# Kernel optimization log

Hardware: AMD Instinct MI355X
Metric: run time of the kernel (lower is better)

## Reference

```python
import jax, jax.numpy as jnp
import numpy as np

B, T1, T2, V, D, H = 128, 256, 256, 50000, 300, 300


def _lstm_dir(x, lens, Wih, Whh, bih, bhh):
    # PyTorch LSTM gate order: i, f, g, o. Length-masked scan emulates pack_padded_sequence:
    # state frozen and outputs zeroed for t >= len.
    Bn, T, _ = x.shape
    Hn = Whh.shape[1]
    mask = (jnp.arange(T)[None, :] < lens[:, None]).astype(x.dtype)[..., None]  # [B,T,1]

    def step(carry, inp):
        h, c = carry
        xt, mt = inp
        gates = xt @ Wih.T + bih + h @ Whh.T + bhh
        i, f, g, o = jnp.split(gates, 4, axis=-1)
        c_new = jax.nn.sigmoid(f) * c + jax.nn.sigmoid(i) * jnp.tanh(g)
        h_new = jax.nn.sigmoid(o) * jnp.tanh(c_new)
        h = mt * h_new + (1.0 - mt) * h
        c = mt * c_new + (1.0 - mt) * c
        return (h, c), h * mt

    init = (jnp.zeros((Bn, Hn), x.dtype), jnp.zeros((Bn, Hn), x.dtype))
    _, ys = jax.lax.scan(step, init, (x.swapaxes(0, 1), mask.swapaxes(0, 1)))
    return ys.swapaxes(0, 1)  # [B,T,H]


def _bilstm(x, lens, Wf_ih, Wf_hh, bf_ih, bf_hh, Wb_ih, Wb_hh, bb_ih, bb_hh):
    out_f = _lstm_dir(x, lens, Wf_ih, Wf_hh, bf_ih, bf_hh)
    T = x.shape[1]
    t = jnp.arange(T)[None, :]
    # per-sample reversal of the valid prefix (involution): rev[t] = l-1-t for t<l else t
    idx = jnp.where(t < lens[:, None], lens[:, None] - 1 - t, t)
    xr = jnp.take_along_axis(x, idx[..., None], axis=1)
    yr = _lstm_dir(xr, lens, Wb_ih, Wb_hh, bb_ih, bb_hh)
    out_b = jnp.take_along_axis(yr, idx[..., None], axis=1)
    return jnp.concatenate([out_f, out_b], axis=-1)  # [B,T,2H]


def _bidaf_both(u1, l1, u2, l2):
    S = jnp.einsum('bid,bjd->bij', u1, u2)  # [B,t1,t2]
    v1 = jnp.arange(S.shape[1])[None, :] < l1[:, None]
    v2 = jnp.arange(S.shape[2])[None, :] < l2[:, None]
    Sm = jnp.where(v1[:, :, None] & v2[:, None, :], S, -1e9)
    # softmax over t2 (s1->s2 attention); invalid rows zeroed (matches NaN->0 fill)
    a2 = jax.nn.softmax(Sm, axis=2) * v1[:, :, None].astype(S.dtype)
    a1 = jax.nn.softmax(Sm, axis=1) * v2[:, None, :].astype(S.dtype)
    U = jnp.einsum('bij,bjd->bid', a2, u2)   # tile for s1
    U1 = jnp.einsum('bij,bid->bjd', a1, u1)  # tile for s2
    return U, U1


def _max_along_time(x, lens):
    v = jnp.arange(x.shape[1])[None, :] < lens[:, None]
    return jnp.max(jnp.where(v[:, :, None], x, -jnp.inf), axis=1)


def _forward(s1, l1, s2, l2, emb,
             w1f_ih, w1f_hh, b1f_ih, b1f_hh, w1b_ih, w1b_hh, b1b_ih, b1b_hh,
             w2f_ih, w2f_hh, b2f_ih, b2f_hh, w2b_ih, w2b_hh, b2b_ih, b2b_hh,
             projW, projB, mlpW, mlpB, smW, smB):
    p1 = emb[s1]  # [B,T1,D]
    p2 = emb[s2]
    u1 = _bilstm(p1, l1, w1f_ih, w1f_hh, b1f_ih, b1f_hh, w1b_ih, w1b_hh, b1b_ih, b1b_hh)
    u2 = _bilstm(p2, l2, w1f_ih, w1f_hh, b1f_ih, b1f_hh, w1b_ih, w1b_hh, b1b_ih, b1b_hh)
    A1, A2 = _bidaf_both(u1, l1, u2, l2)
    c1 = jnp.concatenate([u1, A1, u1 - A1, u1 * A1], axis=-1)  # [B,T1,8H]
    c2 = jnp.concatenate([u2, A2, u2 - A2, u2 * A2], axis=-1)
    p1c = jax.nn.relu(c1 @ projW.T + projB)
    p2c = jax.nn.relu(c2 @ projW.T + projB)
    y1 = _bilstm(p1c, l1, w2f_ih, w2f_hh, b2f_ih, b2f_hh, w2b_ih, w2b_hh, b2b_ih, b2b_hh)
    y2 = _bilstm(p2c, l2, w2f_ih, w2f_hh, b2f_ih, b2f_hh, w2b_ih, w2b_hh, b2b_ih, b2b_hh)
    m1 = _max_along_time(y1, l1)  # [B,2H]
    m2 = _max_along_time(y2, l2)
    feat = jnp.concatenate([m1, m2, jnp.abs(m1 - m2), m1 * m2], axis=-1)  # [B,8H]
    h = jax.nn.relu(feat @ mlpW.T + mlpB)
    return h @ smW.T + smB  # [B,3]


def setup_inputs():
    key = jax.random.key(0)
    ks = jax.random.split(key, 24)
    sc = 0.05
    W = lambda i, shape: jax.random.normal(ks[i], shape, jnp.float32) * sc
    return dict(
        s1=jax.random.randint(ks[0], (B, T1), 0, V),
        l1=jax.random.randint(ks[1], (B,), 1, T1 + 1),
        s2=jax.random.randint(ks[2], (B, T2), 0, V),
        l2=jax.random.randint(ks[3], (B,), 1, T2 + 1),
        emb=W(4, (V, D)),
        w1f_ih=W(5, (4 * H, D)), w1f_hh=W(6, (4 * H, H)), b1f_ih=W(7, (4 * H,)), b1f_hh=W(8, (4 * H,)),
        w1b_ih=W(9, (4 * H, D)), w1b_hh=W(10, (4 * H, H)), b1b_ih=W(11, (4 * H,)), b1b_hh=W(12, (4 * H,)),
        w2f_ih=W(13, (4 * H, H)), w2f_hh=W(14, (4 * H, H)), b2f_ih=W(15, (4 * H,)), b2f_hh=W(16, (4 * H,)),
        w2b_ih=W(17, (4 * H, H)), w2b_hh=W(18, (4 * H, H)), b2b_ih=W(19, (4 * H,)), b2b_hh=W(20, (4 * H,)),
        projW=W(21, (H, 8 * H)), projB=jnp.zeros((H,), jnp.float32),
        mlpW=W(22, (300, 8 * H)), mlpB=jnp.zeros((300,), jnp.float32),
        smW=W(23, (3, 300)), smB=jnp.zeros((3,), jnp.float32),
    )


def reference(s1, l1, s2, l2, emb,
              w1f_ih, w1f_hh, b1f_ih, b1f_hh, w1b_ih, w1b_hh, b1b_ih, b1b_hh,
              w2f_ih, w2f_hh, b2f_ih, b2f_hh, w2b_ih, w2b_hh, b2b_ih, b2b_hh,
              projW, projB, mlpW, mlpB, smW, smB):
    return _forward(s1, l1, s2, l2, emb,
                    w1f_ih, w1f_hh, b1f_ih, b1f_hh, w1b_ih, w1b_hh, b1b_ih, b1b_hh,
                    w2f_ih, w2f_hh, b2f_ih, b2f_hh, w2b_ih, w2b_hh, b2b_ih, b2b_hh,
                    projW, projB, mlpW, mlpB, smW, smB)
```

## Files before the change

kernel.cpp:

```cpp
#include <hip/hip_runtime.h>
#include <hip/hip_bf16.h>


typedef unsigned short u16;
typedef float fx4 __attribute__((ext_vector_type(4)));
typedef short s16x8 __attribute__((ext_vector_type(8)));

__device__ __forceinline__ float us2f(u16 u){
  unsigned int x = ((unsigned int)u) << 16;
  float f; __builtin_memcpy(&f, &x, 4); return f;
}
__device__ __forceinline__ u16 f2us(float f){
  unsigned int x; __builtin_memcpy(&x, &f, 4);
  unsigned int r = x + 0x7fffu + ((x >> 16) & 1u);
  return (u16)(r >> 16);
}
__device__ __forceinline__ float sigmf(float x){ return 1.0f/(1.0f + __expf(-x)); }
__device__ __forceinline__ float tanhfast(float x){ return 1.0f - 2.0f/(__expf(2.0f*x) + 1.0f); }

__global__ __launch_bounds__(256) void k_embed(const int* __restrict__ s1, const int* __restrict__ s2,
                                               const float* __restrict__ emb, u16* __restrict__ p)
{
  int id = blockIdx.x*256 + threadIdx.x;
  if (id >= 65536*75) return;
  int row = id / 75;
  int c4 = (id - row*75) * 4;
  int tok = (row < 32768) ? s1[row] : s2[row - 32768];
  float4 v = *(const float4*)(emb + (size_t)tok*300 + c4);
  ushort4 o; o.x=f2us(v.x); o.y=f2us(v.y); o.z=f2us(v.z); o.w=f2us(v.w);
  *(ushort4*)(p + (size_t)row*300 + c4) = o;
}

__global__ __launch_bounds__(256) void k_cvt(const float* __restrict__ in, u16* __restrict__ out, int n)
{
  int id = blockIdx.x*256 + threadIdx.x;
  if (id < n) out[id] = f2us(in[id]);
}

__global__ __launch_bounds__(256) void k_pack(const float* __restrict__ W, u16* __restrict__ pack)
{
  int id = blockIdx.x*256 + threadIdx.x;
  if (id >= 51200) return;
  const int lane = id & 63;
  const int kt2 = (id >> 6) % 10;
  const int nt2 = id / 640;
  const int n = nt2*16 + (lane & 15);
  u16 tmp[8];
#pragma unroll
  for (int j = 0; j < 8; ++j){
    const int k = kt2*32 + (lane >> 4)*8 + j;
    tmp[j] = (n < 1200 && k < 300) ? f2us(W[(size_t)n*300 + k]) : (u16)0;
  }
  *(s16x8*)(pack + (size_t)id*8) = *(const s16x8*)tmp;
}

__global__ __launch_bounds__(256) void k_mm_xpc(
    const u16* __restrict__ A,
    const u16* __restrict__ WFb, const u16* __restrict__ WBb,
    const float* __restrict__ bF1, const float* __restrict__ bF2,
    const float* __restrict__ bB1, const float* __restrict__ bB2,
    const int* __restrict__ l1, const int* __restrict__ l2,
    u16* __restrict__ xp, int c)
{
  const int dir = blockIdx.z;
  const u16* Bw = dir ? WBb : WFb;
  const float* b1 = dir ? bB1 : bF1;
  const float* b2 = dir ? bB2 : bF2;
  u16* xpd = xp + (size_t)dir*9830400;
  __shared__ u16 As[128][40];
  __shared__ u16 Bs[128][40];
  const int tid = threadIdx.x;
  const int m0 = blockIdx.y << 7;
  const int n0 = blockIdx.x << 7;
  const int srow0 = tid >> 2;
  const int kcol = (tid & 3) << 3;
  int src[2];
#pragma unroll
  for (int p = 0; p < 2; ++p){
    const int row = srow0 + (p << 6);
    const int ml = m0 + row;
    const int r = ml >> 5, tl = ml & 31;
    const int L = (r < 128) ? l1[r] : l2[r-128];
    const int tg = (c << 5) + tl;
    const int s = dir ? ((tg < L) ? (L-1-tg) : tg) : tg;
    src[p] = r*256 + s;
  }
  const int wv = tid >> 6;
  const int wm = (wv >> 1) << 6, wn = (wv & 1) << 6;
  const int lq = (tid >> 4) & 3;
  const int lr = tid & 15;
  fx4 acc[4][4];
#pragma unroll
  for (int i = 0; i < 4; ++i)
#pragma unroll
    for (int j = 0; j < 4; ++j) acc[i][j] = (fx4){0.f,0.f,0.f,0.f};

  for (int kt = 0; kt < 10; ++kt){
    const int k = (kt << 5) + kcol;
#pragma unroll
    for (int p = 0; p < 2; ++p){
      u16 tmp[8];
      const u16* ap = A + (size_t)src[p]*300 + k;
      if (k + 8 <= 300){
        *(ushort4*)&tmp[0] = *(const ushort4*)ap;
        *(ushort4*)&tmp[4] = *(const ushort4*)(ap + 4);
      } else {
#pragma unroll
        for (int j = 0; j < 8; ++j) tmp[j] = (k + j < 300) ? ap[j] : (u16)0;
      }
      *(s16x8*)&As[srow0 + (p << 6)][kcol] = *(const s16x8*)tmp;

      const int n = n0 + srow0 + (p << 6);
      u16 tmb[8] = {0,0,0,0,0,0,0,0};
      if (n < 1200){
        const u16* bp = Bw + (size_t)n*300 + k;
        if (k + 8 <= 300){
          *(ushort4*)&tmb[0] = *(const ushort4*)bp;
          *(ushort4*)&tmb[4] = *(const ushort4*)(bp + 4);
        } else {
#pragma unroll
          for (int j = 0; j < 8; ++j) tmb[j] = (k + j < 300) ? bp[j] : (u16)0;
        }
      }
      *(s16x8*)&Bs[srow0 + (p << 6)][kcol] = *(const s16x8*)tmb;
    }
    __syncthreads();
    s16x8 af[4], bf[4];
#pragma unroll
    for (int mi = 0; mi < 4; ++mi) af[mi] = *(const s16x8*)&As[wm + mi*16 + lr][lq << 3];
#pragma unroll
    for (int ni = 0; ni < 4; ++ni) bf[ni] = *(const s16x8*)&Bs[wn + ni*16 + lr][lq << 3];
#pragma unroll
    for (int mi = 0; mi < 4; ++mi)
#pragma unroll
      for (int ni = 0; ni < 4; ++ni)
        acc[mi][ni] = __builtin_amdgcn_mfma_f32_16x16x32_bf16(af[mi], bf[ni], acc[mi][ni], 0, 0, 0);
    __syncthreads();
  }
#pragma unroll
  for (int ni = 0; ni < 4; ++ni){
    const int n = n0 + wn + ni*16 + lr;
    if (n < 1200){
      const float bias = b1[n] + b2[n];
#pragma unroll
      for (int mi = 0; mi < 4; ++mi){
        const int m = m0 + wm + mi*16 + (lq << 2);
#pragma unroll
        for (int reg = 0; reg < 4; ++reg)
          xpd[(size_t)(m + reg)*1200 + n] = f2us(acc[mi][ni][reg] + bias);
      }
    }
  }
}

__global__ __launch_bounds__(256) void k_mm_s(const u16* __restrict__ U, float* __restrict__ S)
{
  __shared__ u16 As[128][40];
  __shared__ u16 Bs[128][40];
  const int tid = threadIdx.x;
  const int bz = blockIdx.z;
  const u16* Ap = U + (size_t)bz*153600;
  const u16* Bp = U + (size_t)(128+bz)*153600;
  float* C = S + (size_t)bz*65536;
  const int m0 = blockIdx.y << 7;
  const int n0 = blockIdx.x << 7;
  const int srow0 = tid >> 2;
  const int kcol = (tid & 3) << 3;
  const int wv = tid >> 6;
  const int wm = (wv >> 1) << 6, wn = (wv & 1) << 6;
  const int lq = (tid >> 4) & 3;
  const int lr = tid & 15;
  fx4 acc[4][4];
#pragma unroll
  for (int i = 0; i < 4; ++i)
#pragma unroll
    for (int j = 0; j < 4; ++j) acc[i][j] = (fx4){0.f,0.f,0.f,0.f};

  for (int kt = 0; kt < 19; ++kt){
    const int k = (kt << 5) + kcol;
#pragma unroll
    for (int p = 0; p < 2; ++p){
      const int row = srow0 + (p << 6);
      u16 tma[8] = {0,0,0,0,0,0,0,0};
      u16 tmb[8] = {0,0,0,0,0,0,0,0};
      if (k + 8 <= 600){
        *(s16x8*)tma = *(const s16x8*)(Ap + (size_t)(m0 + row)*600 + k);
        *(s16x8*)tmb = *(const s16x8*)(Bp + (size_t)(n0 + row)*600 + k);
      }
      *(s16x8*)&As[row][kcol] = *(const s16x8*)tma;
      *(s16x8*)&Bs[row][kcol] = *(const s16x8*)tmb;
    }
    __syncthreads();
    s16x8 af[4], bf[4];
#pragma unroll
    for (int mi = 0; mi < 4; ++mi) af[mi] = *(const s16x8*)&As[wm + mi*16 + lr][lq << 3];
#pragma unroll
    for (int ni = 0; ni < 4; ++ni) bf[ni] = *(const s16x8*)&Bs[wn + ni*16 + lr][lq << 3];
#pragma unroll
    for (int mi = 0; mi < 4; ++mi)
#pragma unroll
      for (int ni = 0; ni < 4; ++ni)
        acc[mi][ni] = __builtin_amdgcn_mfma_f32_16x16x32_bf16(af[mi], bf[ni], acc[mi][ni], 0, 0, 0);
    __syncthreads();
  }
#pragma unroll
  for (int mi = 0; mi < 4; ++mi){
    const int m = m0 + wm + mi*16 + (lq << 2);
#pragma unroll
    for (int ni = 0; ni < 4; ++ni){
      const int n = n0 + wn + ni*16 + lr;
#pragma unroll
      for (int reg = 0; reg < 4; ++reg)
        C[(size_t)(m + reg)*256 + n] = acc[mi][ni][reg];
    }
  }
}

__global__ __launch_bounds__(256) void k_mm_proj(
    const u16* __restrict__ U, const u16* __restrict__ ATT,
    const u16* __restrict__ Bw,
    const float* __restrict__ bias,
    u16* __restrict__ C)
{
  __shared__ u16 As0[128][40];
  __shared__ u16 As1[128][40];
  __shared__ u16 Bs0[128][40];
  __shared__ u16 Bs1[128][40];
  const int tid = threadIdx.x;
  const int id = ((int)(blockIdx.x & 7))*192 + ((int)blockIdx.x >> 3);
  const int mg = id / 3, nb = id - mg*3;
  const int m0 = mg << 7, n0 = nb << 7;
  const int srow0 = tid >> 2;
  const int kcol = (tid & 3) << 3;
  const int wv = tid >> 6;
  const int wm = (wv >> 1) << 6, wn = (wv & 1) << 6;
  const int lq = (tid >> 4) & 3;
  const int lr = tid & 15;
  fx4 acc[4][4];
#pragma unroll
  for (int i = 0; i < 4; ++i)
#pragma unroll
    for (int j = 0; j < 4; ++j) acc[i][j] = (fx4){0.f,0.f,0.f,0.f};

  for (int kt = 0; kt < 19; ++kt){
    const int off = (kt << 5) + kcol;
    const bool ok = (off < 600);
#pragma unroll
    for (int p = 0; p < 2; ++p){
      const int row = srow0 + (p << 6);
      u16 u8[8] = {0,0,0,0,0,0,0,0};
      u16 a8[8] = {0,0,0,0,0,0,0,0};
      if (ok){
        *(s16x8*)u8 = *(const s16x8*)(U   + (size_t)(m0+row)*600 + off);
        *(s16x8*)a8 = *(const s16x8*)(ATT + (size_t)(m0+row)*600 + off);
      }
      *(s16x8*)&As0[row][kcol] = *(const s16x8*)u8;
      *(s16x8*)&As1[row][kcol] = *(const s16x8*)a8;
      const int n = n0 + row;
      u16 w0[8] = {0,0,0,0,0,0,0,0};
      u16 w1[8] = {0,0,0,0,0,0,0,0};
      if (n < 300 && ok){
        *(s16x8*)w0 = *(const s16x8*)(Bw + (size_t)n*2400 + off);
        *(s16x8*)w1 = *(const s16x8*)(Bw + (size_t)n*2400 + 600 + off);
      }
      *(s16x8*)&Bs0[row][kcol] = *(const s16x8*)w0;
      *(s16x8*)&Bs1[row][kcol] = *(const s16x8*)w1;
    }
    __syncthreads();
    {
      s16x8 af0[4], af1[4], bf0[4], bf1[4];
#pragma unroll
      for (int mi = 0; mi < 4; ++mi){
        af0[mi] = *(const s16x8*)&As0[wm + mi*16 + lr][lq << 3];
        af1[mi] = *(const s16x8*)&As1[wm + mi*16 + lr][lq << 3];
      }
#pragma unroll
      for (int ni = 0; ni < 4; ++ni){
        bf0[ni] = *(const s16x8*)&Bs0[wn + ni*16 + lr][lq << 3];
        bf1[ni] = *(const s16x8*)&Bs1[wn + ni*16 + lr][lq << 3];
      }
#pragma unroll
      for (int mi = 0; mi < 4; ++mi)
#pragma unroll
        for (int ni = 0; ni < 4; ++ni){
          acc[mi][ni] = __builtin_amdgcn_mfma_f32_16x16x32_bf16(af0[mi], bf0[ni], acc[mi][ni], 0, 0, 0);
          acc[mi][ni] = __builtin_amdgcn_mfma_f32_16x16x32_bf16(af1[mi], bf1[ni], acc[mi][ni], 0, 0, 0);
        }
    }
    __syncthreads();
#pragma unroll
    for (int p = 0; p < 2; ++p){
      const int row = srow0 + (p << 6);
      u16 u8[8] = {0,0,0,0,0,0,0,0};
      u16 a8[8] = {0,0,0,0,0,0,0,0};
      if (ok){
        *(s16x8*)u8 = *(const s16x8*)(U   + (size_t)(m0+row)*600 + off);
        *(s16x8*)a8 = *(const s16x8*)(ATT + (size_t)(m0+row)*600 + off);
      }
      u16 d8[8], m8[8];
#pragma unroll
      for (int j = 0; j < 8; ++j){
        const float uf = us2f(u8[j]), af = us2f(a8[j]);
        d8[j] = f2us(uf - af);
        m8[j] = f2us(uf * af);
      }
      *(s16x8*)&As0[row][kcol] = *(const s16x8*)d8;
      *(s16x8*)&As1[row][kcol] = *(const s16x8*)m8;
      const int n = n0 + row;
      u16 w2[8] = {0,0,0,0,0,0,0,0};
      u16 w3[8] = {0,0,0,0,0,0,0,0};
      if (n < 300 && ok){
        *(s16x8*)w2 = *(const s16x8*)(Bw + (size_t)n*2400 + 1200 + off);
        *(s16x8*)w3 = *(const s16x8*)(Bw + (size_t)n*2400 + 1800 + off);
      }
      *(s16x8*)&Bs0[row][kcol] = *(const s16x8*)w2;
      *(s16x8*)&Bs1[row][kcol] = *(const s16x8*)w3;
    }
    __syncthreads();
    {
      s16x8 af0[4], af1[4], bf0[4], bf1[4];
#pragma unroll
      for (int mi = 0; mi < 4; ++mi){
        af0[mi] = *(const s16x8*)&As0[wm + mi*16 + lr][lq << 3];
        af1[mi] = *(const s16x8*)&As1[wm + mi*16 + lr][lq << 3];
      }
#pragma unroll
      for (int ni = 0; ni < 4; ++ni){
        bf0[ni] = *(const s16x8*)&Bs0[wn + ni*16 + lr][lq << 3];
        bf1[ni] = *(const s16x8*)&Bs1[wn + ni*16 + lr][lq << 3];
      }
#pragma unroll
      for (int mi = 0; mi < 4; ++mi)
#pragma unroll
        for (int ni = 0; ni < 4; ++ni){
          acc[mi][ni] = __builtin_amdgcn_mfma_f32_16x16x32_bf16(af0[mi], bf0[ni], acc[mi][ni], 0, 0, 0);
          acc[mi][ni] = __builtin_amdgcn_mfma_f32_16x16x32_bf16(af1[mi], bf1[ni], acc[mi][ni], 0, 0, 0);
        }
    }
    __syncthreads();
  }
#pragma unroll
  for (int ni = 0; ni < 4; ++ni){
    const int n = n0 + wn + ni*16 + lr;
    if (n < 300){
      const float bs = bias[n];
#pragma unroll
      for (int mi = 0; mi < 4; ++mi){
        const int m = m0 + wm + mi*16 + (lq << 2);
#pragma unroll
        for (int reg = 0; reg < 4; ++reg)
          C[(size_t)(m + reg)*300 + n] = f2us(fmaxf(acc[mi][ni][reg] + bs, 0.0f));
      }
    }
  }
}

__global__ __launch_bounds__(512) void k_scan_mf(
    const u16* __restrict__ xp,
    const u16* __restrict__ packF, const u16* __restrict__ packB,
    const int* __restrict__ l1, const int* __restrict__ l2,
    u16* __restrict__ uo,
    u16* __restrict__ hG, float* __restrict__ cG,
    int c)
{
  __shared__ u16 h_s[16][328];
  __shared__ float c_s[8][304];
  __shared__ float gs[8][1200];
  __shared__ u16 xstage[8][1200];
  __shared__ u16 wring[8][2][5][512];
  __shared__ int L_s[8];
  const int bid = blockIdx.x;
  const int dir = bid & 1, sg = bid >> 1;
  const int r0 = sg << 3;
  const u16* pack = dir ? packB : packF;
  const u16* xpd = xp + (size_t)dir*9830400;
  const int tid = threadIdx.x;
  if (tid < 8) L_s[tid] = (r0 + tid < 128) ? l1[r0 + tid] : l2[r0 + tid - 128];
  for (int i = tid; i < 16*328; i += 512){
    const int q = i / 328, d = i - q*328;
    u16 v = 0;
    if (q < 8 && c > 0) v = hG[(size_t)(dir*256 + r0 + q)*328 + d];
    h_s[q][d] = v;
  }
  for (int i = tid; i < 8*304; i += 512){
    const int q = i / 304, d = i - q*304;
    c_s[q][d] = (c > 0) ? cG[(size_t)(dir*256 + r0 + q)*304 + d] : 0.0f;
  }
  const int w = tid >> 6, lane = tid & 63;
  const int lq = lane >> 4, lr = lane & 15;
  const int tile0 = w * 10;
  const u16* pw = pack + (size_t)tile0*5120;
  const unsigned wbase = (unsigned)(uintptr_t)&wring[w][0][0][0] + (unsigned)lane*16u;

  int xq[3], xc[3]; bool xv[3];
#pragma unroll
  for (int j = 0; j < 3; ++j){
    const int i = tid + (j << 9);
    xv[j] = (i < 1200);
    const int qq = (i < 1200) ? (i / 150) : 0;
    xq[j] = qq;
    xc[j] = (i - qq*150) * 8;
  }
#pragma unroll
  for (int j = 0; j < 3; ++j){
    if (xv[j]){
      s16x8 v = *(const s16x8*)(xpd + (size_t)((r0 + xq[j])*32 + 0)*1200 + xc[j]);
      *(s16x8*)&xstage[xq[j]][xc[j]] = v;
    }
  }
  __syncthreads();
  int Lmax = 0;
#pragma unroll
  for (int q = 0; q < 8; ++q) Lmax = max(Lmax, L_s[q]);
  const int t0 = c << 5;
  int nts = Lmax - t0; if (nts > 32) nts = 32;
  if (nts <= 0) return;

#define WISSUE(PH)                                                                       \
  {                                                                                      \
    const int buf_ = (PH) & 1, kt_ = (PH) >> 1, hh_ = (PH) & 1;                          \
    _Pragma("unroll")                                                                    \
    for (int nt2 = 0; nt2 < 5; ++nt2){                                                   \
      const u16* ga = pw + ((size_t)((hh_*5 + nt2)*10 + kt_))*512 + (size_t)lane*8;      \
      __builtin_amdgcn_global_load_lds(                                                  \
        (const __attribute__((address_space(1))) void*)ga,                               \
        (__attribute__((address_space(3))) void*)&wring[w][buf_][nt2][0], 16, 0, 0);     \
    }                                                                                    \
  }

  WISSUE(0)
  WISSUE(1)

  for (int tl = 0; tl < nts; ++tl){
    const int t = t0 + tl;
    const bool pf = (tl + 1 < nts);
    s16x8 xr0, xr1, xr2;
    if (pf){
      if (xv[0]) xr0 = *(const s16x8*)(xpd + (size_t)((r0 + xq[0])*32 + tl + 1)*1200 + xc[0]);
      if (xv[1]) xr1 = *(const s16x8*)(xpd + (size_t)((r0 + xq[1])*32 + tl + 1)*1200 + xc[1]);
      if (xv[2]) xr2 = *(const s16x8*)(xpd + (size_t)((r0 + xq[2])*32 + tl + 1)*1200 + xc[2]);
    }
    fx4 acc[10];
#pragma unroll
    for (int nt = 0; nt < 10; ++nt) acc[nt] = (fx4){0.f,0.f,0.f,0.f};

#pragma unroll
    for (int ph = 0; ph < 20; ++ph){
      const int kt = ph >> 1, hh = ph & 1, buf = ph & 1;
      asm volatile("s_waitcnt vmcnt(5)" ::: "memory");
      __builtin_amdgcn_sched_barrier(0);
      const unsigned ab = wbase + (unsigned)(buf*5)*1024u;
      s16x8 b0, b1, b2, b3, b4;
      asm volatile("ds_read_b128 %0, %1"             : "=v"(b0) : "v"(ab));
      asm volatile("ds_read_b128 %0, %1 offset:1024" : "=v"(b1) : "v"(ab));
      asm volatile("ds_read_b128 %0, %1 offset:2048" : "=v"(b2) : "v"(ab));
      asm volatile("ds_read_b128 %0, %1 offset:3072" : "=v"(b3) : "v"(ab));
      asm volatile("ds_read_b128 %0, %1 offset:4096" : "=v"(b4) : "v"(ab));
      const s16x8 a = *(const s16x8*)&h_s[lr][kt*32 + (lq << 3)];
      asm volatile("s_waitcnt lgkmcnt(0)" ::: "memory");
      __builtin_amdgcn_sched_barrier(0);
      acc[hh*5+0] = __builtin_amdgcn_mfma_f32_16x16x32_bf16(a, b0, acc[hh*5+0], 0, 0, 0);
      acc[hh*5+1] = __builtin_amdgcn_mfma_f32_16x16x32_bf16(a, b1, acc[hh*5+1], 0, 0, 0);
      acc[hh*5+2] = __builtin_amdgcn_mfma_f32_16x16x32_bf16(a, b2, acc[hh*5+2], 0, 0, 0);
      acc[hh*5+3] = __builtin_amdgcn_mfma_f32_16x16x32_bf16(a, b3, acc[hh*5+3], 0, 0, 0);
      acc[hh*5+4] = __builtin_amdgcn_mfma_f32_16x16x32_bf16(a, b4, acc[hh*5+4], 0, 0, 0);
      WISSUE((ph + 2) % 20)
    }
    if (lq < 2){
#pragma unroll
      for (int nt = 0; nt < 10; ++nt){
        const int n = (tile0 + nt)*16 + lr;
        if (n < 1200){
#pragma unroll
          for (int reg = 0; reg < 4; ++reg)
            gs[(lq << 2) + reg][n] = acc[nt][reg];
        }
      }
    }
    asm volatile("s_waitcnt lgkmcnt(0)" ::: "memory");
    __builtin_amdgcn_sched_barrier(0);
    __builtin_amdgcn_s_barrier();
#pragma unroll
    for (int j = 0; j < 5; ++j){
      const int u0 = tid + (j << 9);
      if (u0 < 2400){
        const int q = u0 / 300, d = u0 - q*300;
        const int L = L_s[q];
        if (t < L){
          const float gi = gs[q][d]       + us2f(xstage[q][d]);
          const float gf = gs[q][300 + d] + us2f(xstage[q][300 + d]);
          const float gg = gs[q][600 + d] + us2f(xstage[q][600 + d]);
          const float go = gs[q][900 + d] + us2f(xstage[q][900 + d]);
          const float cn = sigmf(gf)*c_s[q][d] + sigmf(gi)*tanhfast(gg);
          const float hn = sigmf(go)*tanhfast(cn);
          c_s[q][d] = cn;
          const u16 hb = f2us(hn);
          h_s[q][d] = hb;
          const int wpos = dir ? (L-1-t) : t;
          uo[(size_t)((r0 + q)*256 + wpos)*600 + dir*300 + d] = hb;
        }
      }
    }
    asm volatile("s_waitcnt lgkmcnt(0)" ::: "memory");
    __builtin_amdgcn_sched_barrier(0);
    __builtin_amdgcn_s_barrier();
    if (pf){
      if (xv[0]) *(s16x8*)&xstage[xq[0]][xc[0]] = xr0;
      if (xv[1]) *(s16x8*)&xstage[xq[1]][xc[1]] = xr1;
      if (xv[2]) *(s16x8*)&xstage[xq[2]][xc[2]] = xr2;
    }
  }
#undef WISSUE
  for (int i = tid; i < 8*328; i += 512){
    const int q = i / 328, d = i - q*328;
    hG[(size_t)(dir*256 + r0 + q)*328 + d] = h_s[q][d];
  }
  for (int i = tid; i < 8*304; i += 512){
    const int q = i / 304, d = i - q*304;
    cG[(size_t)(dir*256 + r0 + q)*304 + d] = c_s[q][d];
  }
}

__global__ __launch_bounds__(256) void k_row_stats(const float* __restrict__ S, const int* __restrict__ l2,
                                                   float* __restrict__ rmax, float* __restrict__ rinv)
{
  const int wid = threadIdx.x >> 6, lane = threadIdx.x & 63;
  const int row = blockIdx.x*4 + wid;
  const int b = row >> 8;
  const int L2b = l2[b];
  float4 v = *(const float4*)(S + (size_t)row*256 + lane*4);
  const int j = lane*4;
  float m = -INFINITY;
  if (j   < L2b) m = fmaxf(m, v.x);
  if (j+1 < L2b) m = fmaxf(m, v.y);
  if (j+2 < L2b) m = fmaxf(m, v.z);
  if (j+3 < L2b) m = fmaxf(m, v.w);
  for (int off = 32; off; off >>= 1) m = fmaxf(m, __shfl_xor(m, off));
  float s = 0.f;
  if (j   < L2b) s += __expf(v.x - m);
  if (j+1 < L2b) s += __expf(v.y - m);
  if (j+2 < L2b) s += __expf(v.z - m);
  if (j+3 < L2b) s += __expf(v.w - m);
  for (int off = 32; off; off >>= 1) s += __shfl_xor(s, off);
  if (lane == 0){ rmax[row] = m; rinv[row] = 1.0f/s; }
}

__global__ __launch_bounds__(256) void k_col_stats(const float* __restrict__ S, const int* __restrict__ l1,
                                                   float* __restrict__ cmax, float* __restrict__ cinv)
{
  const int b = blockIdx.x;
  const int j = threadIdx.x;
  const int L1b = l1[b];
  const float* Sb = S + (size_t)b*65536;
  float m = -INFINITY;
  for (int i = 0; i < L1b; ++i) m = fmaxf(m, Sb[(size_t)i*256 + j]);
  float s = 0.f;
  for (int i = 0; i < L1b; ++i) s += __expf(Sb[(size_t)i*256 + j] - m);
  cmax[b*256 + j] = m;
  cinv[b*256 + j] = 1.0f/s;
}

__global__ __launch_bounds__(256) void k_av_row(
    const float* __restrict__ S, const u16* __restrict__ U,
    const int* __restrict__ l1, const int* __restrict__ l2,
    const float* __restrict__ rmax, const float* __restrict__ rinv,
    u16* __restrict__ ATT)
{
  __shared__ float Ps[32][68];
  __shared__ float Us[32][68];
  const int tid = threadIdx.x;
  const int b = blockIdx.z;
  const int i0 = blockIdx.y << 6;
  const int d0 = blockIdx.x << 6;
  const int L1b = l1[b], L2b = l2[b];
  const float* Sb = S + (size_t)b*65536;
  const u16* u2 = U + (size_t)(128+b)*153600;
  const int tx = tid & 15, ty = tid >> 4;
  float acc[4][4];
#pragma unroll
  for (int i = 0; i < 4; ++i)
#pragma unroll
    for (int j = 0; j < 4; ++j) acc[i][j] = 0.0f;

  for (int kt = 0; kt < 8; ++kt){
    const int j0 = kt << 5;
#pragma unroll
    for (int q = 0; q < 2; ++q){
      const int f4 = tid + (q << 8);
      {
        const int row = f4 >> 3;
        const int c4 = (f4 & 7) << 2;
        const int i = i0 + row;
        float4 s4 = *(const float4*)(Sb + (size_t)i*256 + j0 + c4);
        const float rm = rmax[(b<<8) + i];
        const float ri = rinv[(b<<8) + i];
        const int jb = j0 + c4;
        Ps[c4  ][row] = (jb   < L2b) ? __expf(s4.x - rm)*ri : 0.0f;
        Ps[c4+1][row] = (jb+1 < L2b) ? __expf(s4.y - rm)*ri : 0.0f;
        Ps[c4+2][row] = (jb+2 < L2b) ? __expf(s4.z - rm)*ri : 0.0f;
        Ps[c4+3][row] = (jb+3 < L2b) ? __expf(s4.w - rm)*ri : 0.0f;
      }
      {
        const int row = f4 >> 4;
        const int c4 = (f4 & 15) << 2;
        const int d = d0 + c4;
        float4 v = make_float4(0.f,0.f,0.f,0.f);
        if (j0 + row < L2b){
          const u16* up = u2 + (size_t)(j0+row)*600 + d;
          if (d + 3 < 600){
            ushort4 t4 = *(const ushort4*)up;
            v.x=us2f(t4.x); v.y=us2f(t4.y); v.z=us2f(t4.z); v.w=us2f(t4.w);
          } else {
            if (d   < 600) v.x = us2f(up[0]);
            if (d+1 < 600) v.y = us2f(up[1]);
            if (d+2 < 600) v.z = us2f(up[2]);
          }
        }
        *(float4*)&Us[row][c4] = v;
      }
    }
    __syncthreads();
#pragma unroll
    for (int kk = 0; kk < 32; ++kk){
      float4 a = *(const float4*)&Ps[kk][ty<<2];
      float4 bb = *(const float4*)&Us[kk][tx<<2];
      float av[4] = {a.x,a.y,a.z,a.w};
      float bv[4] = {bb.x,bb.y,bb.z,bb.w};
#pragma unroll
      for (int ii = 0; ii < 4; ++ii)
#pragma unroll
        for (int jj = 0; jj < 4; ++jj)
          acc[ii][jj] = fmaf(av[ii], bv[jj], acc[ii][jj]);
    }
    __syncthreads();
  }
#pragma unroll
  for (int ii = 0; ii < 4; ++ii){
    const int i = i0 + (ty<<2) + ii;
#pragma unroll
    for (int jj = 0; jj < 4; ++jj){
      const int d = d0 + (tx<<2) + jj;
      if (d < 600)
        ATT[(size_t)b*153600 + (size_t)i*600 + d] = f2us((i < L1b) ? acc[ii][jj] : 0.0f);
    }
  }
}

__global__ __launch_bounds__(256) void k_av_col(
    const float* __restrict__ S, const u16* __restrict__ U,
    const int* __restrict__ l1, const int* __restrict__ l2,
    const float* __restrict__ cmax, const float* __restrict__ cinv,
    u16* __restrict__ ATT)
{
  __shared__ float Ps[32][68];
  __shared__ float Us[32][68];
  const int tid = threadIdx.x;
  const int b = blockIdx.z;
  const int j0v = blockIdx.y << 6;
  const int d0 = blockIdx.x << 6;
  const int L1b = l1[b], L2b = l2[b];
  const float* Sb = S + (size_t)b*65536;
  const u16* u1 = U + (size_t)b*153600;
  const int tx = tid & 15, ty = tid >> 4;
  float acc[4][4];
#pragma unroll
  for (int i = 0; i < 4; ++i)
#pragma unroll
    for (int j = 0; j < 4; ++j) acc[i][j] = 0.0f;

  for (int kt = 0; kt < 8; ++kt){
    const int i0k = kt << 5;
#pragma unroll
    for (int q = 0; q < 2; ++q){
      const int f4 = tid + (q << 8);
      const int row = f4 >> 4;
      const int c4 = (f4 & 15) << 2;
      {
        const int i = i0k + row;
        const int j = j0v + c4;
        float4 s4 = *(const float4*)(Sb + (size_t)i*256 + j);
        const bool iok = i < L1b;
        Ps[row][c4  ] = iok ? __expf(s4.x - cmax[(b<<8)+j  ])*cinv[(b<<8)+j  ] : 0.0f;
        Ps[row][c4+1] = iok ? __expf(s4.y - cmax[(b<<8)+j+1])*cinv[(b<<8)+j+1] : 0.0f;
        Ps[row][c4+2] = iok ? __expf(s4.z - cmax[(b<<8)+j+2])*cinv[(b<<8)+j+2] : 0.0f;
        Ps[row][c4+3] = iok ? __expf(s4.w - cmax[(b<<8)+j+3])*cinv[(b<<8)+j+3] : 0.0f;
      }
      {
        const int d = d0 + c4;
        float4 v = make_float4(0.f,0.f,0.f,0.f);
        if (i0k + row < L1b){
          const u16* up = u1 + (size_t)(i0k+row)*600 + d;
          if (d + 3 < 600){
            ushort4 t4 = *(const ushort4*)up;
            v.x=us2f(t4.x); v.y=us2f(t4.y); v.z=us2f(t4.z); v.w=us2f(t4.w);
          } else {
            if (d   < 600) v.x = us2f(up[0]);
            if (d+1 < 600) v.y = us2f(up[1]);
            if (d+2 < 600) v.z = us2f(up[2]);
          }
        }
        *(float4*)&Us[row][c4] = v;
      }
    }
    __syncthreads();
#pragma unroll
    for (int kk = 0; kk < 32; ++kk){
      float4 a = *(const float4*)&Ps[kk][ty<<2];
      float4 bb = *(const float4*)&Us[kk][tx<<2];
      float av[4] = {a.x,a.y,a.z,a.w};
      float bv[4] = {bb.x,bb.y,bb.z,bb.w};
#pragma unroll
      for (int ii = 0; ii < 4; ++ii)
#pragma unroll
        for (int jj = 0; jj < 4; ++jj)
          acc[ii][jj] = fmaf(av[ii], bv[jj], acc[ii][jj]);
    }
    __syncthreads();
  }
#pragma unroll
  for (int ii = 0; ii < 4; ++ii){
    const int j = j0v + (ty<<2) + ii;
#pragma unroll
    for (int jj = 0; jj < 4; ++jj){
      const int d = d0 + (tx<<2) + jj;
      if (d < 600)
        ATT[(size_t)(128+b)*153600 + (size_t)j*600 + d] = f2us((j < L2b) ? acc[ii][jj] : 0.0f);
    }
  }
}

__global__ __launch_bounds__(256) void k_maxfeat(const u16* __restrict__ y,
                                                 const int* __restrict__ l1, const int* __restrict__ l2,
                                                 float* __restrict__ feat)
{
  const int b = blockIdx.x;
  const int La = l1[b], Lb = l2[b];
  for (int c = threadIdx.x; c < 600; c += 256){
    float m1 = -INFINITY, m2 = -INFINITY;
    const u16* y1 = y + (size_t)b*153600 + c;
    for (int t = 0; t < La; ++t) m1 = fmaxf(m1, us2f(y1[(size_t)t*600]));
    const u16* y2 = y + (size_t)(128+b)*153600 + c;
    for (int t = 0; t < Lb; ++t) m2 = fmaxf(m2, us2f(y2[(size_t)t*600]));
    feat[(size_t)b*2400 + c]        = m1;
    feat[(size_t)b*2400 + 600 + c]  = m2;
    feat[(size_t)b*2400 + 1200 + c] = fabsf(m1 - m2);
    feat[(size_t)b*2400 + 1800 + c] = m1*m2;
  }
}

__global__ __launch_bounds__(256) void k_rowgemm(const float* __restrict__ feat, const float* __restrict__ W,
                                                 const float* __restrict__ bias, float* __restrict__ out)
{
  const int b = blockIdx.x;
  __shared__ float ff[2400];
  for (int i = threadIdx.x; i < 2400; i += 256) ff[i] = feat[(size_t)b*2400 + i];
  __syncthreads();
  for (int n = threadIdx.x; n < 300; n += 256){
    const float* w = W + (size_t)n*2400;
    float acc = bias[n];
    for (int k = 0; k < 2400; k += 4){
      float4 wv = *(const float4*)(w + k);
      acc += ff[k]*wv.x + ff[k+1]*wv.y + ff[k+2]*wv.z + ff[k+3]*wv.w;
    }
    out[(size_t)b*300 + n] = fmaxf(acc, 0.0f);
  }
}

__global__ __launch_bounds__(192) void k_final(const float* __restrict__ h, const float* __restrict__ smW,
                                               const float* __restrict__ smB, float* __restrict__ out)
{
  const int b = blockIdx.x;
  const int n = threadIdx.x >> 6, lane = threadIdx.x & 63;
  float acc = 0.f;
  for (int k = lane; k < 300; k += 64) acc += h[(size_t)b*300 + k]*smW[(size_t)n*300 + k];
  for (int off = 32; off; off >>= 1) acc += __shfl_xor(acc, off);
  if (lane == 0) out[b*3 + n] = acc + smB[n];
}

extern "C" void kernel_launch(void* const* d_in, const int* in_sizes, int n_in,
                              void* d_out, int out_size, void* d_ws, size_t ws_size,
                              hipStream_t stream)
{
  (void)in_sizes; (void)n_in; (void)out_size;
  static const size_t OFF_P  = 0;
  static const size_t OFF_B  = 39321600;
  static const size_t OFF_U  = 78643200;
  static const size_t OFF_D  = 157286400;
  static const size_t OFF_WT = 235929600;
  static const size_t OFF_PJ = 238809600;
  static const size_t OFF_PK = 240249600;
  static const size_t OFF_ST = 243526400;
  static const size_t OFF_FE = 244050688;
  static const size_t OFF_HM = 245279488;
  static const size_t OFF_HC = 245433088;
  static const size_t WS_NEEDED = 246391552;
  if (ws_size < WS_NEEDED) return;

  const int* s1 = (const int*)d_in[0];
  const int* l1 = (const int*)d_in[1];
  const int* s2 = (const int*)d_in[2];
  const int* l2 = (const int*)d_in[3];
  const float* emb    = (const float*)d_in[4];
  const float* w1f_ih = (const float*)d_in[5];
  const float* w1f_hh = (const float*)d_in[6];
  const float* b1f_ih = (const float*)d_in[7];
  const float* b1f_hh = (const float*)d_in[8];
  const float* w1b_ih = (const float*)d_in[9];
  const float* w1b_hh = (const float*)d_in[10];
  const float* b1b_ih = (const float*)d_in[11];
  const float* b1b_hh = (const float*)d_in[12];
  const float* w2f_ih = (const float*)d_in[13];
  const float* w2f_hh = (const float*)d_in[14];
  const float* b2f_ih = (const float*)d_in[15];
  const float* b2f_hh = (const float*)d_in[16];
  const float* w2b_ih = (const float*)d_in[17];
  const float* w2b_hh = (const float*)d_in[18];
  const float* b2b_ih = (const float*)d_in[19];
  const float* b2b_hh = (const float*)d_in[20];
  const float* projW  = (const float*)d_in[21];
  const float* projB  = (const float*)d_in[22];
  const float* mlpW   = (const float*)d_in[23];
  const float* mlpB   = (const float*)d_in[24];
  const float* smW    = (const float*)d_in[25];
  const float* smB    = (const float*)d_in[26];

  char* ws = (char*)d_ws;
  u16*   p    = (u16*)(ws + OFF_P);
  u16*   xp1  = (u16*)(ws + OFF_B);
  float* Smat = (float*)(ws + OFF_B);
  u16*   pc   = (u16*)(ws + OFF_B);
  u16*   uu   = (u16*)(ws + OFF_U);
  u16*   att  = (u16*)(ws + OFF_D);
  u16*   xp2  = (u16*)(ws + OFF_D);
  u16*   wih  = (u16*)(ws + OFF_WT);
  u16*   pjw  = (u16*)(ws + OFF_PJ);
  u16*   pk   = (u16*)(ws + OFF_PK);
  float* st   = (float*)(ws + OFF_ST);
  float* feat = (float*)(ws + OFF_FE);
  float* hml  = (float*)(ws + OFF_HM);
  u16*   hG   = (u16*)(ws + OFF_HC);
  float* cG   = (float*)(ws + OFF_HC + 335872);

  k_embed<<<19200, 256, 0, stream>>>(s1, s2, emb, p);
  k_cvt<<<1407, 256, 0, stream>>>(w1f_ih, wih,           360000);
  k_cvt<<<1407, 256, 0, stream>>>(w1b_ih, wih + 360000,  360000);
  k_cvt<<<1407, 256, 0, stream>>>(w2f_ih, wih + 720000,  360000);
  k_cvt<<<1407, 256, 0, stream>>>(w2b_ih, wih + 1080000, 360000);
  k_cvt<<<2813, 256, 0, stream>>>(projW,  pjw,           720000);
  k_pack<<<200, 256, 0, stream>>>(w1f_hh, pk);
  k_pack<<<200, 256, 0, stream>>>(w1b_hh, pk + 409600);
  k_pack<<<200, 256, 0, stream>>>(w2f_hh, pk + 819200);
  k_pack<<<200, 256, 0, stream>>>(w2b_hh, pk + 1228800);

  const dim3 gxp(10, 64, 2);
  for (int c = 0; c < 8; ++c){
    k_mm_xpc<<<gxp, 256, 0, stream>>>(p, wih, wih + 360000, b1f_ih, b1f_hh, b1b_ih, b1b_hh,
                                      l1, l2, xp1, c);
    k_scan_mf<<<64, 512, 0, stream>>>(xp1, pk, pk + 409600, l1, l2, uu, hG, cG, c);
  }

  k_mm_s<<<dim3(2,2,128), 256, 0, stream>>>(uu, Smat);
  k_row_stats<<<8192, 256, 0, stream>>>(Smat, l2, st, st + 32768);
  k_col_stats<<<128, 256, 0, stream>>>(Smat, l1, st + 65536, st + 98304);
  k_av_row<<<dim3(10,4,128), 256, 0, stream>>>(Smat, uu, l1, l2, st, st + 32768, att);
  k_av_col<<<dim3(10,4,128), 256, 0, stream>>>(Smat, uu, l1, l2, st + 65536, st + 98304, att);

  k_mm_proj<<<1536, 256, 0, stream>>>(uu, att, pjw, projB, pc);

  for (int c = 0; c < 8; ++c){
    k_mm_xpc<<<gxp, 256, 0, stream>>>(pc, wih + 720000, wih + 1080000, b2f_ih, b2f_hh, b2b_ih, b2b_hh,
                                      l1, l2, xp2, c);
    k_scan_mf<<<64, 512, 0, stream>>>(xp2, pk + 819200, pk + 1228800, l1, l2, uu, hG, cG, c);
  }

  k_maxfeat<<<128, 256, 0, stream>>>(uu, l1, l2, feat);
  k_rowgemm<<<128, 256, 0, stream>>>(feat, mlpW, mlpB, hml);
  k_final<<<128, 192, 0, stream>>>(hml, smW, smB, (float*)d_out);
}
```

Baseline: 9.026 ms.

## Restructure LSTM scan kernel: packed h layout, triple-buffered weights, register cell state

Reworks the recurrent LSTM scan kernel. The hidden state is stored in an MFMA-fragment-packed LDS layout, and the weight stream moves from a 2-deep ring of 5 tiles to a 3-deep ring of 4 tiles, giving a 25-phase flat loop with more loads in flight. The cell state now lives in registers instead of LDS, and input projections are gathered directly from global memory each step instead of being staged in LDS. The aim is lower LDS footprint, fewer LDS round-trips, and better hiding of weight-load latency, at the cost of scalar global gathers on the critical path of each step.

```diff
diff --git a/kernel.cpp b/kernel.cpp
--- a/kernel.cpp
+++ b/kernel.cpp
@@ -363,11 +363,9 @@
     u16* __restrict__ hG, float* __restrict__ cG,
     int c)
 {
-  __shared__ u16 h_s[16][328];
-  __shared__ float c_s[8][304];
+  __shared__ u16 h_pack[10][64][8];
   __shared__ float gs[8][1200];
-  __shared__ u16 xstage[8][1200];
-  __shared__ u16 wring[8][2][5][512];
+  __shared__ u16 wring[8][3][4][512];
   __shared__ int L_s[8];
   const int bid = blockIdx.x;
   const int dir = bid & 1, sg = bid >> 1;
@@ -376,96 +374,109 @@
   const u16* xpd = xp + (size_t)dir*9830400;
   const int tid = threadIdx.x;
   if (tid < 8) L_s[tid] = (r0 + tid < 128) ? l1[r0 + tid] : l2[r0 + tid - 128];
-  for (int i = tid; i < 16*328; i += 512){
-    const int q = i / 328, d = i - q*328;
-    u16 v = 0;
-    if (q < 8 && c > 0) v = hG[(size_t)(dir*256 + r0 + q)*328 + d];
-    h_s[q][d] = v;
-  }
-  for (int i = tid; i < 8*304; i += 512){
-    const int q = i / 304, d = i - q*304;
-    c_s[q][d] = (c > 0) ? cG[(size_t)(dir*256 + r0 + q)*304 + d] : 0.0f;
-  }
+  for (int i = tid; i < 10*64*8; i += 512) ((u16*)h_pack)[i] = 0;
+  __syncthreads();
+  if (c > 0){
+    for (int i = tid; i < 2400; i += 512){
+      const int q = i / 300, d = i - q*300;
+      h_pack[d >> 5][(((d & 31) >> 3) << 4) | q][d & 7] =
+          hG[(size_t)(dir*256 + r0 + q)*328 + d];
+    }
+  }
+  int q_[5], d_[5]; bool v_[5];
+#pragma unroll
+  for (int j = 0; j < 5; ++j){
+    const int u0 = tid + (j << 9);
+    v_[j] = (u0 < 2400);
+    const int qq = v_[j] ? (u0 / 300) : 0;
+    q_[j] = qq;
+    d_[j] = v_[j] ? (u0 - qq*300) : 0;
+  }
+  float c_reg[5];
+#pragma unroll
+  for (int j = 0; j < 5; ++j)
+    c_reg[j] = (v_[j] && c > 0) ? cG[(size_t)(dir*256 + r0 + q_[j])*304 + d_[j]] : 0.0f;
+  __syncthreads();
+
+  int Lmax = 0;
+#pragma unroll
+  for (int q = 0; q < 8; ++q) Lmax = max(Lmax, L_s[q]);
+  const int t0 = c << 5;
+  int nts = Lmax - t0; if (nts > 32) nts = 32;
+  if (nts <= 0) return;
+
   const int w = tid >> 6, lane = tid & 63;
   const int lq = lane >> 4, lr = lane & 15;
   const int tile0 = w * 10;
   const u16* pw = pack + (size_t)tile0*5120;
-  const unsigned wbase = (unsigned)(uintptr_t)&wring[w][0][0][0] + (unsigned)lane*16u;
-
-  int xq[3], xc[3]; bool xv[3];
-#pragma unroll
-  for (int j = 0; j < 3; ++j){
-    const int i = tid + (j << 9);
-    xv[j] = (i < 1200);
-    const int qq = (i < 1200) ? (i / 150) : 0;
-    xq[j] = qq;
-    xc[j] = (i - qq*150) * 8;
-  }
-#pragma unroll
-  for (int j = 0; j < 3; ++j){
-    if (xv[j]){
-      s16x8 v = *(const s16x8*)(xpd + (size_t)((r0 + xq[j])*32 + 0)*1200 + xc[j]);
-      *(s16x8*)&xstage[xq[j]][xc[j]] = v;
-    }
-  }
-  __syncthreads();
-  int Lmax = 0;
-#pragma unroll
-  for (int q = 0; q < 8; ++q) Lmax = max(Lmax, L_s[q]);
-  const int t0 = c << 5;
-  int nts = Lmax - t0; if (nts > 32) nts = 32;
-  if (nts <= 0) return;
-
-#define WISSUE(PH)                                                                       \
+  const unsigned wb0 = (unsigned)(uintptr_t)&wring[w][0][0][0] + (unsigned)lane*16u;
+
+#define WISSUE(FB, BUF)                                                                  \
   {                                                                                      \
-    const int buf_ = (PH) & 1, kt_ = (PH) >> 1, hh_ = (PH) & 1;                          \
     _Pragma("unroll")                                                                    \
-    for (int nt2 = 0; nt2 < 5; ++nt2){                                                   \
-      const u16* ga = pw + ((size_t)((hh_*5 + nt2)*10 + kt_))*512 + (size_t)lane*8;      \
+    for (int i2 = 0; i2 < 4; ++i2){                                                      \
+      const int f_ = (FB) + i2;                                                          \
+      const u16* ga = pw + ((size_t)(((f_ % 10)*10) + (f_ / 10)))*512 + (size_t)lane*8;  \
       __builtin_amdgcn_global_load_lds(                                                  \
         (const __attribute__((address_space(1))) void*)ga,                               \
-        (__attribute__((address_space(3))) void*)&wring[w][buf_][nt2][0], 16, 0, 0);     \
+        (__attribute__((address_space(3))) void*)&wring[w][BUF][i2][0], 16, 0, 0);       \
     }                                                                                    \
   }
 
-  WISSUE(0)
-  WISSUE(1)
+  WISSUE(0, 0)
+  WISSUE(4, 1)
+  int rot = 0;
 
   for (int tl = 0; tl < nts; ++tl){
     const int t = t0 + tl;
-    const bool pf = (tl + 1 < nts);
-    s16x8 xr0, xr1, xr2;
-    if (pf){
-      if (xv[0]) xr0 = *(const s16x8*)(xpd + (size_t)((r0 + xq[0])*32 + tl + 1)*1200 + xc[0]);
-      if (xv[1]) xr1 = *(const s16x8*)(xpd + (size_t)((r0 + xq[1])*32 + tl + 1)*1200 + xc[1]);
-      if (xv[2]) xr2 = *(const s16x8*)(xpd + (size_t)((r0 + xq[2])*32 + tl + 1)*1200 + xc[2]);
-    }
+    const int bsel0 = rot;
+    const int bsel1 = (rot + 1 == 3) ? 0 : rot + 1;
+    const int bsel2 = (rot + 2 >= 3) ? rot - 1 : rot + 2;
+    const int bsel[3] = { bsel0, bsel1, bsel2 };
+    __builtin_amdgcn_sched_barrier(0);
+    u16 xg0[5], xg1[5], xg2[5], xg3[5];
+#pragma unroll
+    for (int j = 0; j < 5; ++j){
+      const size_t base = (size_t)((r0 + q_[j])*32 + tl)*1200 + d_[j];
+      xg0[j] = v_[j] ? xpd[base      ] : (u16)0;
+      xg1[j] = v_[j] ? xpd[base + 300] : (u16)0;
+      xg2[j] = v_[j] ? xpd[base + 600] : (u16)0;
+      xg3[j] = v_[j] ? xpd[base + 900] : (u16)0;
+    }
+    __builtin_amdgcn_sched_barrier(0);
+
     fx4 acc[10];
 #pragma unroll
     for (int nt = 0; nt < 10; ++nt) acc[nt] = (fx4){0.f,0.f,0.f,0.f};
 
 #pragma unroll
-    for (int ph = 0; ph < 20; ++ph){
-      const int kt = ph >> 1, hh = ph & 1, buf = ph & 1;
-      asm volatile("s_waitcnt vmcnt(5)" ::: "memory");
+    for (int p = 0; p < 25; ++p){
+      if (p < 2){ asm volatile("s_waitcnt vmcnt(24)" ::: "memory"); }
+      else      { asm volatile("s_waitcnt vmcnt(4)"  ::: "memory"); }
       __builtin_amdgcn_sched_barrier(0);
-      const unsigned ab = wbase + (unsigned)(buf*5)*1024u;
-      s16x8 b0, b1, b2, b3, b4;
+      const unsigned ab = wb0 + (unsigned)bsel[p % 3]*4096u;
+      s16x8 b0, b1, b2, b3;
       asm volatile("ds_read_b128 %0, %1"             : "=v"(b0) : "v"(ab));
       asm volatile("ds_read_b128 %0, %1 offset:1024" : "=v"(b1) : "v"(ab));
       asm volatile("ds_read_b128 %0, %1 offset:2048" : "=v"(b2) : "v"(ab));
       asm volatile("ds_read_b128 %0, %1 offset:3072" : "=v"(b3) : "v"(ab));
-      asm volatile("ds_read_b128 %0, %1 offset:4096" : "=v"(b4) : "v"(ab));
-      const s16x8 a = *(const s16x8*)&h_s[lr][kt*32 + (lq << 3)];
+      const int kt0 = (4*p) / 10;
+      const int kt3 = (4*p + 3) / 10;
+      const s16x8 a0 = *(const s16x8*)&h_pack[kt0][lane][0];
+      const s16x8 a1 = (kt3 != kt0) ? *(const s16x8*)&h_pack[kt3][lane][0] : a0;
+      WISSUE((((p + 2) % 25) * 4), bsel[(p + 2) % 3])
       asm volatile("s_waitcnt lgkmcnt(0)" ::: "memory");
       __builtin_amdgcn_sched_barrier(0);
-      acc[hh*5+0] = __builtin_amdgcn_mfma_f32_16x16x32_bf16(a, b0, acc[hh*5+0], 0, 0, 0);
-      acc[hh*5+1] = __builtin_amdgcn_mfma_f32_16x16x32_bf16(a, b1, acc[hh*5+1], 0, 0, 0);
-      acc[hh*5+2] = __builtin_amdgcn_mfma_f32_16x16x32_bf16(a, b2, acc[hh*5+2], 0, 0, 0);
-      acc[hh*5+3] = __builtin_amdgcn_mfma_f32_16x16x32_bf16(a, b3, acc[hh*5+3], 0, 0, 0);
-      acc[hh*5+4] = __builtin_amdgcn_mfma_f32_16x16x32_bf16(a, b4, acc[hh*5+4], 0, 0, 0);
-      WISSUE((ph + 2) % 20)
-    }
+      {
+        const int f0 = 4*p;
+        acc[(f0+0) % 10] = __builtin_amdgcn_mfma_f32_16x16x32_bf16(((f0+0)/10 == kt0) ? a0 : a1, b0, acc[(f0+0) % 10], 0, 0, 0);
+        acc[(f0+1) % 10] = __builtin_amdgcn_mfma_f32_16x16x32_bf16(((f0+1)/10 == kt0) ? a0 : a1, b1, acc[(f0+1) % 10], 0, 0, 0);
+        acc[(f0+2) % 10] = __builtin_amdgcn_mfma_f32_16x16x32_bf16(((f0+2)/10 == kt0) ? a0 : a1, b2, acc[(f0+2) % 10], 0, 0, 0);
+        acc[(f0+3) % 10] = __builtin_amdgcn_mfma_f32_16x16x32_bf16(((f0+3)/10 == kt0) ? a0 : a1, b3, acc[(f0+3) % 10], 0, 0, 0);
+      }
+    }
+    rot = (rot + 1 == 3) ? 0 : rot + 1;
+
     if (lq < 2){
 #pragma unroll
       for (int nt = 0; nt < 10; ++nt){
@@ -482,20 +493,19 @@
     __builtin_amdgcn_s_barrier();
 #pragma unroll
     for (int j = 0; j < 5; ++j){
-      const int u0 = tid + (j << 9);
-      if (u0 < 2400){
-        const int q = u0 / 300, d = u0 - q*300;
+      if (v_[j]){
+        const int q = q_[j], d = d_[j];
         const int L = L_s[q];
         if (t < L){
-          const float gi = gs[q][d]       + us2f(xstage[q][d]);
-          const float gf = gs[q][300 + d] + us2f(xstage[q][300 + d]);
-          const float gg = gs[q][600 + d] + us2f(xstage[q][600 + d]);
-          const float go = gs[q][900 + d] + us2f(xstage[q][900 + d]);
-          const float cn = sigmf(gf)*c_s[q][d] + sigmf(gi)*tanhfast(gg);
+          const float gi = gs[q][d]       + us2f(xg0[j]);
+          const float gf = gs[q][300 + d] + us2f(xg1[j]);
+          const float gg = gs[q][600 + d] + us2f(xg2[j]);
+          const float go = gs[q][900 + d] + us2f(xg3[j]);
+          const float cn = sigmf(gf)*c_reg[j] + sigmf(gi)*tanhfast(gg);
           const float hn = sigmf(go)*tanhfast(cn);
-          c_s[q][d] = cn;
+          c_reg[j] = cn;
           const u16 hb = f2us(hn);
-          h_s[q][d] = hb;
+          h_pack[d >> 5][(((d & 31) >> 3) << 4) | q][d & 7] = hb;
           const int wpos = dir ? (L-1-t) : t;
           uo[(size_t)((r0 + q)*256 + wpos)*600 + dir*300 + d] = hb;
         }
@@ -504,21 +514,16 @@
     asm volatile("s_waitcnt lgkmcnt(0)" ::: "memory");
     __builtin_amdgcn_sched_barrier(0);
     __builtin_amdgcn_s_barrier();
-    if (pf){
-      if (xv[0]) *(s16x8*)&xstage[xq[0]][xc[0]] = xr0;
-      if (xv[1]) *(s16x8*)&xstage[xq[1]][xc[1]] = xr1;
-      if (xv[2]) *(s16x8*)&xstage[xq[2]][xc[2]] = xr2;
-    }
   }
 #undef WISSUE
-  for (int i = tid; i < 8*328; i += 512){
-    const int q = i / 328, d = i - q*328;
-    hG[(size_t)(dir*256 + r0 + q)*328 + d] = h_s[q][d];
-  }
-  for (int i = tid; i < 8*304; i += 512){
-    const int q = i / 304, d = i - q*304;
-    cG[(size_t)(dir*256 + r0 + q)*304 + d] = c_s[q][d];
-  }
+  for (int i = tid; i < 2400; i += 512){
+    const int q = i / 300, d = i - q*300;
+    hG[(size_t)(dir*256 + r0 + q)*328 + d] =
+        h_pack[d >> 5][(((d & 31) >> 3) << 4) | q][d & 7];
+  }
+#pragma unroll
+  for (int j = 0; j < 5; ++j)
+    if (v_[j]) cG[(size_t)(dir*256 + r0 + q_[j])*304 + d_[j]] = c_reg[j];
 }
 
 __global__ __launch_bounds__(256) void k_row_stats(const float* __restrict__ S, const int* __restrict__ l2,
```

Result: slower. 9.869 ms (+9.3%).
